# Performance work log

Hardware: AMD Instinct MI355X
Metric: run time of the kernel (lower is better)

The kernel has to match this reference:

```python
import jax, jax.numpy as jnp
import numpy as np

DEPTH = 11          # tree depth
D = 1024            # input_width
H = 32              # hidden_width (leaf MLP)
O = 1024            # output_width
B = 4096            # flattened token batch
N_LEAVES = 2 ** DEPTH
N_NODES = 2 ** DEPTH - 1


def setup_inputs() -> dict:
    key = jax.random.key(0)
    ks = jax.random.split(key, 7)
    f1 = 1.0 / np.sqrt(D)
    f2 = 1.0 / np.sqrt(H)
    u = lambda k, shape, f: jax.random.uniform(k, shape, jnp.float32, -f, f)
    return {
        "x": jax.random.normal(ks[0], (B, D), jnp.float32),
        "node_weights": u(ks[1], (N_NODES, D), f1),
        "node_biases": u(ks[2], (N_NODES,), f1),   # (n_nodes,1) in torch; flattened
        "w1s": u(ks[3], (N_LEAVES, D, H), f1),
        "b1s": u(ks[4], (N_LEAVES, H), f1),
        "w2s": u(ks[5], (N_LEAVES, H, O), f2),
        "b2s": u(ks[6], (N_LEAVES, O), f2),
    }


def reference(x, node_weights, node_biases, w1s, b1s, w2s, b2s):
    # --- hard tree descent (eval_forward) ---
    nodes = jnp.zeros((x.shape[0],), jnp.int32)
    for i in range(DEPTH):  # fixed small loop over tree depth
        w = node_weights[nodes]                       # [B, D] gathered plane coeffs
        b = node_biases[nodes]                        # [B]
        score = jnp.einsum('bd,bd->b', x, w) + b      # per-sample dot product
        choice = (score >= 0).astype(jnp.int32)
        platform = 2 ** i - 1
        next_platform = 2 ** (i + 1) - 1
        nodes = (nodes - platform) * 2 + choice + next_platform
    leaves = nodes - (2 ** DEPTH - 1)                 # [B] leaf index per sample

    # --- per-sample leaf MLP with gathered weights ---
    h = jax.nn.relu(jnp.einsum('bd,bdh->bh', x, w1s[leaves]) + b1s[leaves])  # [B, H]
    out = jnp.einsum('bh,bho->bo', h, w2s[leaves]) + b2s[leaves]             # [B, O]
    return out
```

## Files before the change

### kernel.cpp

```cpp
#include <hip/hip_runtime.h>

#define DEPTH 11
#define D 1024
#define H 32
#define OW 1024
#define B 4096
#define N_LEAVES 2048
#define N_NODES 2047
#define SMAX 4

__global__ __launch_bounds__(256) void descent_kernel(
    const float* __restrict__ x, const float* __restrict__ nw,
    const float* __restrict__ nb, int* __restrict__ leaf,
    int* __restrict__ rnk, int* __restrict__ count)
{
    int lane = threadIdx.x & 63;
    int wv   = threadIdx.x >> 6;
    int samp = blockIdx.x * 4 + wv;

    const float4* xp = (const float4*)(x + (size_t)samp * D);
    float4 xf[4];
#pragma unroll
    for (int k = 0; k < 4; k++) xf[k] = xp[lane + 64 * k];

    int node = 0;
#pragma unroll
    for (int i = 0; i < DEPTH; i++) {
        const float4* wp = (const float4*)(nw + (size_t)node * D);
        double s = 0.0;
#pragma unroll
        for (int k = 0; k < 4; k++) {
            float4 wf = wp[lane + 64 * k];
            s += (double)xf[k].x * (double)wf.x;
            s += (double)xf[k].y * (double)wf.y;
            s += (double)xf[k].z * (double)wf.z;
            s += (double)xf[k].w * (double)wf.w;
        }
#pragma unroll
        for (int m = 32; m >= 1; m >>= 1) s += __shfl_xor(s, m, 64);
        double score = s + (double)nb[node];
        int choice = (score >= 0.0) ? 1 : 0;
        node = 2 * node + 1 + choice;
    }
    int lf = node - N_NODES;
    if (lane == 0) {
        leaf[samp] = lf;
        rnk[samp]  = atomicAdd(&count[lf], 1);
    }
}

__global__ __launch_bounds__(256) void scan_kernel(
    const int* __restrict__ count, int* __restrict__ offsets)
{
    __shared__ int tot[256];
    int t = threadIdx.x;
    int c[8], s = 0;
#pragma unroll
    for (int k = 0; k < 8; k++) { c[k] = count[t * 8 + k]; s += c[k]; }
    tot[t] = s;
    __syncthreads();
    for (int off = 1; off < 256; off <<= 1) {
        int v = (t >= off) ? tot[t - off] : 0;
        __syncthreads();
        tot[t] += v;
        __syncthreads();
    }
    int base = (t > 0) ? tot[t - 1] : 0;
#pragma unroll
    for (int k = 0; k < 8; k++) { offsets[t * 8 + k] = base; base += c[k]; }
}

__global__ __launch_bounds__(256) void scatter_kernel(
    const int* __restrict__ leaf, const int* __restrict__ rnk,
    const int* __restrict__ offsets, int* __restrict__ bucket)
{
    int i = blockIdx.x * 256 + threadIdx.x;
    bucket[offsets[leaf[i]] + rnk[i]] = i;
}

template <int SS>
__device__ __forceinline__ void mlp_compute(
    int tid, const float* __restrict__ w1, const float* __restrict__ w2,
    const float* __restrict__ b1, const float* __restrict__ b2,
    float (*xs)[D], float (*pl1)[32][SMAX], float (*hs)[H],
    const int* sidx, float* __restrict__ out)
{
    const int lane = tid & 63, wave = tid >> 6;
    const int jq = tid & 7, dg = tid >> 3;
    const float4* w1v = (const float4*)w1;

    float4 acc[SS];
#pragma unroll
    for (int s = 0; s < SS; s++) acc[s] = make_float4(0.f, 0.f, 0.f, 0.f);

#pragma unroll 8
    for (int k = 0; k < 32; k++) {
        int d = dg + (k << 5);
        float4 w = w1v[(d << 3) + jq];
#pragma unroll
        for (int s = 0; s < SS; s++) {
            float xv = xs[s][d];
            acc[s].x += xv * w.x;
            acc[s].y += xv * w.y;
            acc[s].z += xv * w.z;
            acc[s].w += xv * w.w;
        }
    }
#pragma unroll
    for (int m = 8; m <= 32; m <<= 1)
#pragma unroll
        for (int s = 0; s < SS; s++) {
            acc[s].x += __shfl_xor(acc[s].x, m, 64);
            acc[s].y += __shfl_xor(acc[s].y, m, 64);
            acc[s].z += __shfl_xor(acc[s].z, m, 64);
            acc[s].w += __shfl_xor(acc[s].w, m, 64);
        }
    if (lane < 8) {
#pragma unroll
        for (int s = 0; s < SS; s++) {
            pl1[wave][jq * 4 + 0][s] = acc[s].x;
            pl1[wave][jq * 4 + 1][s] = acc[s].y;
            pl1[wave][jq * 4 + 2][s] = acc[s].z;
            pl1[wave][jq * 4 + 3][s] = acc[s].w;
        }
    }
    __syncthreads();
    if (tid < 32 * SS) {
        int s2 = tid >> 5, j2 = tid & 31;
        float sum = pl1[0][j2][s2] + pl1[1][j2][s2] + pl1[2][j2][s2] +
                    pl1[3][j2][s2] + b1[j2];
        hs[s2][j2] = fmaxf(sum, 0.f);
    }
    __syncthreads();

    const float4* w2v = (const float4*)w2;
    float4 o[SS];
#pragma unroll
    for (int s = 0; s < SS; s++) o[s] = make_float4(0.f, 0.f, 0.f, 0.f);
#pragma unroll 8
    for (int jj = 0; jj < H; jj++) {
        float4 w = w2v[(jj << 8) + tid];
#pragma unroll
        for (int s = 0; s < SS; s++) {
            float hv = hs[s][jj];
            o[s].x += hv * w.x;
            o[s].y += hv * w.y;
            o[s].z += hv * w.z;
            o[s].w += hv * w.w;
        }
    }
    float4 bv = ((const float4*)b2)[tid];
#pragma unroll
    for (int s = 0; s < SS; s++) {
        float4 o4;
        o4.x = o[s].x + bv.x;
        o4.y = o[s].y + bv.y;
        o4.z = o[s].z + bv.z;
        o4.w = o[s].w + bv.w;
        ((float4*)(out + (size_t)sidx[s] * OW))[tid] = o4;
    }
}

__global__ __launch_bounds__(256) void mlp_kernel(
    const float* __restrict__ x, const float* __restrict__ w1s,
    const float* __restrict__ b1s, const float* __restrict__ w2s,
    const float* __restrict__ b2s, const int* __restrict__ offsets,
    const int* __restrict__ count, const int* __restrict__ bucket,
    float* __restrict__ out)
{
    __shared__ float xs[SMAX][D];
    __shared__ float pl1[4][32][SMAX];
    __shared__ float hs[SMAX][H];
    __shared__ int   sidx[SMAX];

    int l  = blockIdx.x;
    int nS = count[l];
    if (nS == 0) return;
    int base = offsets[l];
    int tid  = threadIdx.x;

    const float* w1 = w1s + (size_t)l * D * H;
    const float* w2 = w2s + (size_t)l * H * OW;
    const float* b1 = b1s + (size_t)l * H;
    const float* b2 = b2s + (size_t)l * OW;

    for (int p0 = 0; p0 < nS; p0 += SMAX) {
        int S = min(SMAX, nS - p0);
        if (tid < S) sidx[tid] = bucket[base + p0 + tid];
        __syncthreads();
        for (int s = 0; s < S; s++) {
            ((float4*)xs[s])[tid] = ((const float4*)(x + (size_t)sidx[s] * D))[tid];
        }
        __syncthreads();
        switch (S) {
            case 1: mlp_compute<1>(tid, w1, w2, b1, b2, xs, pl1, hs, sidx, out); break;
            case 2: mlp_compute<2>(tid, w1, w2, b1, b2, xs, pl1, hs, sidx, out); break;
            case 3: mlp_compute<3>(tid, w1, w2, b1, b2, xs, pl1, hs, sidx, out); break;
            default: mlp_compute<4>(tid, w1, w2, b1, b2, xs, pl1, hs, sidx, out); break;
        }
        __syncthreads();
    }
}

extern "C" void kernel_launch(void* const* d_in, const int* in_sizes, int n_in,
                              void* d_out, int out_size, void* d_ws, size_t ws_size,
                              hipStream_t stream)
{
    const float* x   = (const float*)d_in[0];
    const float* nw  = (const float*)d_in[1];
    const float* nb  = (const float*)d_in[2];
    const float* w1s = (const float*)d_in[3];
    const float* b1s = (const float*)d_in[4];
    const float* w2s = (const float*)d_in[5];
    const float* b2s = (const float*)d_in[6];
    float* out = (float*)d_out;

    int* leaf    = (int*)d_ws;
    int* rnk     = leaf + B;
    int* count   = rnk + B;
    int* offsets = count + N_LEAVES;
    int* bucket  = offsets + N_LEAVES;

    hipMemsetAsync(count, 0, N_LEAVES * sizeof(int), stream);
    descent_kernel<<<B / 4, 256, 0, stream>>>(x, nw, nb, leaf, rnk, count);
    scan_kernel<<<1, 256, 0, stream>>>(count, offsets);
    scatter_kernel<<<B / 256, 256, 0, stream>>>(leaf, rnk, offsets, bucket);
    mlp_kernel<<<N_LEAVES, 256, 0, stream>>>(x, w1s, b1s, w2s, b2s,
                                             offsets, count, bucket, out);
}
```

Baseline: 148.8 us.

## Split leaf MLP work into per-chunk items for load balancing

Adds a kernel that builds a compact list of work items, one per group of up to four samples in each non-empty leaf. The MLP kernel then launches one block per item instead of looping over a leaf's samples inside one block. This is meant to spread heavily loaded leaves across blocks and skip empty-leaf blocks. It also sets a launch-bounds occupancy hint. In exchange it adds an extra launch and memset, launches a fixed grid with early exit, and reloads the leaf weights for each chunk of the same leaf.

```diff
diff --git a/kernel.cpp b/kernel.cpp
--- a/kernel.cpp
+++ b/kernel.cpp
@@ -8,6 +8,7 @@
 #define N_LEAVES 2048
 #define N_NODES 2047
 #define SMAX 4
+#define MAX_ITEMS 3072
 
 __global__ __launch_bounds__(256) void descent_kernel(
     const float* __restrict__ x, const float* __restrict__ nw,
@@ -76,6 +77,20 @@
 {
     int i = blockIdx.x * 256 + threadIdx.x;
     bucket[offsets[leaf[i]] + rnk[i]] = i;
+}
+
+__global__ __launch_bounds__(256) void build_items_kernel(
+    const int* __restrict__ count, int* __restrict__ items,
+    int* __restrict__ nitems)
+{
+    int l = blockIdx.x * 256 + threadIdx.x;
+    int c = count[l];
+    if (c > 0) {
+        int k = (c + SMAX - 1) / SMAX;
+        int base = atomicAdd(nitems, k);
+        for (int i = 0; i < k; i++)
+            items[base + i] = l | ((i * SMAX) << 11);
+    }
 }
 
 template <int SS>
@@ -161,11 +176,12 @@
     }
 }
 
-__global__ __launch_bounds__(256) void mlp_kernel(
+__global__ __launch_bounds__(256, 8) void mlp_kernel(
     const float* __restrict__ x, const float* __restrict__ w1s,
     const float* __restrict__ b1s, const float* __restrict__ w2s,
     const float* __restrict__ b2s, const int* __restrict__ offsets,
     const int* __restrict__ count, const int* __restrict__ bucket,
+    const int* __restrict__ items, const int* __restrict__ nitems,
     float* __restrict__ out)
 {
     __shared__ float xs[SMAX][D];
@@ -173,32 +189,30 @@
     __shared__ float hs[SMAX][H];
     __shared__ int   sidx[SMAX];
 
-    int l  = blockIdx.x;
-    int nS = count[l];
-    if (nS == 0) return;
-    int base = offsets[l];
-    int tid  = threadIdx.x;
+    if ((int)blockIdx.x >= nitems[0]) return;
+    int item  = items[blockIdx.x];
+    int l     = item & (N_LEAVES - 1);
+    int start = item >> 11;
+    int S     = min(SMAX, count[l] - start);
+    int base  = offsets[l] + start;
+    int tid   = threadIdx.x;
 
     const float* w1 = w1s + (size_t)l * D * H;
     const float* w2 = w2s + (size_t)l * H * OW;
     const float* b1 = b1s + (size_t)l * H;
     const float* b2 = b2s + (size_t)l * OW;
 
-    for (int p0 = 0; p0 < nS; p0 += SMAX) {
-        int S = min(SMAX, nS - p0);
-        if (tid < S) sidx[tid] = bucket[base + p0 + tid];
-        __syncthreads();
-        for (int s = 0; s < S; s++) {
-            ((float4*)xs[s])[tid] = ((const float4*)(x + (size_t)sidx[s] * D))[tid];
-        }
-        __syncthreads();
-        switch (S) {
-            case 1: mlp_compute<1>(tid, w1, w2, b1, b2, xs, pl1, hs, sidx, out); break;
-            case 2: mlp_compute<2>(tid, w1, w2, b1, b2, xs, pl1, hs, sidx, out); break;
-            case 3: mlp_compute<3>(tid, w1, w2, b1, b2, xs, pl1, hs, sidx, out); break;
-            default: mlp_compute<4>(tid, w1, w2, b1, b2, xs, pl1, hs, sidx, out); break;
-        }
-        __syncthreads();
+    if (tid < S) sidx[tid] = bucket[base + tid];
+    __syncthreads();
+    for (int s = 0; s < S; s++) {
+        ((float4*)xs[s])[tid] = ((const float4*)(x + (size_t)sidx[s] * D))[tid];
+    }
+    __syncthreads();
+    switch (S) {
+        case 1: mlp_compute<1>(tid, w1, w2, b1, b2, xs, pl1, hs, sidx, out); break;
+        case 2: mlp_compute<2>(tid, w1, w2, b1, b2, xs, pl1, hs, sidx, out); break;
+        case 3: mlp_compute<3>(tid, w1, w2, b1, b2, xs, pl1, hs, sidx, out); break;
+        default: mlp_compute<4>(tid, w1, w2, b1, b2, xs, pl1, hs, sidx, out); break;
     }
 }
 
@@ -220,11 +234,16 @@
     int* count   = rnk + B;
     int* offsets = count + N_LEAVES;
     int* bucket  = offsets + N_LEAVES;
+    int* items   = bucket + B;
+    int* nitems  = items + MAX_ITEMS;
 
     hipMemsetAsync(count, 0, N_LEAVES * sizeof(int), stream);
+    hipMemsetAsync(nitems, 0, sizeof(int), stream);
     descent_kernel<<<B / 4, 256, 0, stream>>>(x, nw, nb, leaf, rnk, count);
     scan_kernel<<<1, 256, 0, stream>>>(count, offsets);
     scatter_kernel<<<B / 256, 256, 0, stream>>>(leaf, rnk, offsets, bucket);
-    mlp_kernel<<<N_LEAVES, 256, 0, stream>>>(x, w1s, b1s, w2s, b2s,
-                                             offsets, count, bucket, out);
-}
+    build_items_kernel<<<N_LEAVES / 256, 256, 0, stream>>>(count, items, nitems);
+    mlp_kernel<<<MAX_ITEMS, 256, 0, stream>>>(x, w1s, b1s, w2s, b2s,
+                                              offsets, count, bucket,
+                                              items, nitems, out);
+}
```

New measurement: 143.3 us. -3.7%, faster.
